# Kernel optimization log

Measured on AMD Instinct MI355X. Metric: run time of the kernel, lower is better.

## Reference

```python
import jax, jax.numpy as jnp
import numpy as np

B, N, D, L, T = 64, 64, 6, 32, 2048
RHO = 0.7
W = np.float32(RHO ** (1.0 / L))  # per-step decay, rho ** (1/l_patts)


def setup_inputs() -> dict:
    key = jax.random.key(0)
    k1, k2 = jax.random.split(key)
    x = jax.random.normal(k1, (B, D, T), dtype=jnp.float32)
    patts = jax.random.normal(k2, (N, L), dtype=jnp.float32)  # torch.randn(n_patts, l_patts)
    w = jnp.float32(W)
    return {"x": x, "patts": patts, "w": w}


def _dtw_sq(x, patts, w):
    """Open-end (subsequence) weighted DTW of each pattern against each channel.

    DP recurrence (squared-distance cost, decay w on accumulated path):
      D[0, j] = c[0, j]                                    (free start in time)
      D[i, j] = c[i, j] + w * min(D[i-1, j], D[i, j-1], D[i-1, j-1])
    Output O[b, n, d, j] = D[L-1, j]  (distance of full pattern ending at time j).
    """
    b, d, t = x.shape
    n, l = patts.shape
    is_first = jnp.arange(l) == 0  # (L,)

    def col_step(Dprev_t, xt):
        # Dprev_t: (L, B, N, D) previous time column; xt: (B, D)
        # cost c[i] = (patts[n, i] - x[b, d, j])^2 -> (L, B, N, D)
        c_t = (patts.T[:, None, :, None] - xt[None, :, None, :]) ** 2
        Dprev_im1 = jnp.concatenate(
            [jnp.full_like(Dprev_t[:1], jnp.inf), Dprev_t[:-1]], axis=0)

        def cell(d_im1, inputs):
            ci, dp_i, dp_im1, first = inputs
            m = jnp.minimum(jnp.minimum(dp_i, dp_im1), d_im1)
            di = jnp.where(first, ci, ci + w * m)
            return di, di

        init = jnp.full(Dprev_t.shape[1:], jnp.inf, x.dtype)
        _, Dcol_t = jax.lax.scan(cell, init, (c_t, Dprev_t, Dprev_im1, is_first))
        return Dcol_t, Dcol_t[-1]  # carry full column, emit last row D[L-1, j]

    Dinit = jnp.full((l, b, n, d), jnp.inf, x.dtype)
    xs = jnp.moveaxis(x, -1, 0)  # (T, B, D)
    _, last = jax.lax.scan(col_step, Dinit, xs)  # (T, B, N, D)
    return jnp.moveaxis(last, 0, -1)  # (B, N, D, T)


def reference(x, patts, w):
    return jnp.sqrt(_dtw_sq(x, patts, w))
```

## Files before the change

### kernel.cpp

```cpp
#include <hip/hip_runtime.h>
#include <math.h>

#define TB 2048
#define LL 32
#define NP 64
#define DD 6
#define BB 64
#define NLANES 8
#define ROWS 4
#define PAD 8


template<bool CHECK>
__device__ __forceinline__ void dtw_step(
    int s, int k, bool k0, bool k7,
    const float* __restrict__ xp, float w,
    float p0, float p1, float p2, float p3,
    float& cur0, float& cur1, float& cur2, float& cur3,
    float& diag, float* __restrict__ orow)
{
    const float INF = __builtin_inff();
    float up = __shfl_up(cur3, 1, 64);
    float xv = xp[s];
    int j = s - k;
    bool valid = true;
    if (CHECK) valid = ((unsigned)j < (unsigned)TB);

    float c0 = p0 - xv; c0 *= c0;
    float c1 = p1 - xv; c1 *= c1;
    float c2 = p2 - xv; c2 *= c2;
    float c3 = p3 - xv; c3 *= c3;

    float m0 = fminf(fminf(cur0, up), diag);
    float v0 = k0 ? c0 : fmaf(w, m0, c0);
    float n0 = (CHECK && !valid) ? INF : v0;
    float m1 = fminf(fminf(cur1, n0), cur0);
    float v1 = fmaf(w, m1, c1);
    float n1 = (CHECK && !valid) ? INF : v1;
    float m2 = fminf(fminf(cur2, n1), cur1);
    float v2 = fmaf(w, m2, c2);
    float n2 = (CHECK && !valid) ? INF : v2;
    float m3 = fminf(fminf(cur3, n2), cur2);
    float v3 = fmaf(w, m3, c3);
    float n3 = (CHECK && !valid) ? INF : v3;

    diag = up;
    cur0 = n0; cur1 = n1; cur2 = n2; cur3 = n3;

    if (k7) {
        if (!CHECK || valid) orow[j] = sqrtf(n3);
    }
}

__global__ __launch_bounds__(256) void dtw_kernel(
    const float* __restrict__ x,
    const float* __restrict__ patts,
    const float* __restrict__ wptr,
    float* __restrict__ out)
{
    __shared__ float xs[PAD + TB + PAD];

    const int bid  = blockIdx.x;
    const int half = bid & 1;
    const int bd   = bid >> 1;
    const int b    = bd / DD;
    const int d    = bd - b * DD;
    const int tid  = threadIdx.x;

    const float4* xrow = (const float4*)(x + (size_t)bd * TB);
    float4* xs4 = (float4*)(xs + PAD);
    xs4[tid]       = xrow[tid];
    xs4[tid + 256] = xrow[tid + 256];
    if (tid < PAD) { xs[tid] = 0.f; xs[PAD + TB + tid] = 0.f; }
    __syncthreads();

    const int g = tid >> 3;
    const int k = tid & 7;
    const int n = half * 32 + g;

    const float w = wptr[0];
    const float4 pv = *(const float4*)(patts + n * LL + k * ROWS);
    const float p0 = pv.x, p1 = pv.y, p2 = pv.z, p3 = pv.w;

    float* orow = out + (((size_t)b * NP + n) * DD + d) * TB;
    const float* xp = xs + PAD - k;

    const float INF = __builtin_inff();
    float cur0 = INF, cur1 = INF, cur2 = INF, cur3 = INF, diag = INF;
    const bool k0 = (k == 0), k7 = (k == NLANES - 1);

    int s = 0;
    for (; s < NLANES - 1; ++s)
        dtw_step<true>(s, k, k0, k7, xp, w, p0, p1, p2, p3,
                       cur0, cur1, cur2, cur3, diag, orow);
    #pragma unroll 4
    for (; s < TB; ++s)
        dtw_step<false>(s, k, k0, k7, xp, w, p0, p1, p2, p3,
                        cur0, cur1, cur2, cur3, diag, orow);
    for (; s < TB + NLANES - 1; ++s)
        dtw_step<true>(s, k, k0, k7, xp, w, p0, p1, p2, p3,
                       cur0, cur1, cur2, cur3, diag, orow);
}

extern "C" void kernel_launch(void* const* d_in, const int* in_sizes, int n_in,
                              void* d_out, int out_size, void* d_ws, size_t ws_size,
                              hipStream_t stream) {
    const float* x     = (const float*)d_in[0];
    const float* patts = (const float*)d_in[1];
    const float* wptr  = (const float*)d_in[2];
    float* out = (float*)d_out;

    dim3 grid(BB * DD * 2);
    dim3 block(256);
    dtw_kernel<<<grid, block, 0, stream>>>(x, patts, wptr, out);
}
```

Baseline: 357.0 us.

## Skew DTW wavefront by 16-step time chunks instead of single steps

The lane-to-lane wavefront now advances one 16-column chunk at a time instead of one column at a time. Each chunk's boundary values are exchanged with 16 independent shuffles at its start, so shuffle latency no longer sits on the critical path of every step. Outputs are written as float4 stores. In exchange, pipeline fill and drain grow to seven chunks, adding some redundant compute. Register use also rises because of the 16-entry boundary arrays.

```diff
diff --git a/kernel.cpp b/kernel.cpp
--- a/kernel.cpp
+++ b/kernel.cpp
@@ -8,49 +8,9 @@
 #define BB 64
 #define NLANES 8
 #define ROWS 4
-#define PAD 8
+#define CW 16
+#define MSTEPS (TB/CW)
 
-
-template<bool CHECK>
-__device__ __forceinline__ void dtw_step(
-    int s, int k, bool k0, bool k7,
-    const float* __restrict__ xp, float w,
-    float p0, float p1, float p2, float p3,
-    float& cur0, float& cur1, float& cur2, float& cur3,
-    float& diag, float* __restrict__ orow)
-{
-    const float INF = __builtin_inff();
-    float up = __shfl_up(cur3, 1, 64);
-    float xv = xp[s];
-    int j = s - k;
-    bool valid = true;
-    if (CHECK) valid = ((unsigned)j < (unsigned)TB);
-
-    float c0 = p0 - xv; c0 *= c0;
-    float c1 = p1 - xv; c1 *= c1;
-    float c2 = p2 - xv; c2 *= c2;
-    float c3 = p3 - xv; c3 *= c3;
-
-    float m0 = fminf(fminf(cur0, up), diag);
-    float v0 = k0 ? c0 : fmaf(w, m0, c0);
-    float n0 = (CHECK && !valid) ? INF : v0;
-    float m1 = fminf(fminf(cur1, n0), cur0);
-    float v1 = fmaf(w, m1, c1);
-    float n1 = (CHECK && !valid) ? INF : v1;
-    float m2 = fminf(fminf(cur2, n1), cur1);
-    float v2 = fmaf(w, m2, c2);
-    float n2 = (CHECK && !valid) ? INF : v2;
-    float m3 = fminf(fminf(cur3, n2), cur2);
-    float v3 = fmaf(w, m3, c3);
-    float n3 = (CHECK && !valid) ? INF : v3;
-
-    diag = up;
-    cur0 = n0; cur1 = n1; cur2 = n2; cur3 = n3;
-
-    if (k7) {
-        if (!CHECK || valid) orow[j] = sqrtf(n3);
-    }
-}
 
 __global__ __launch_bounds__(256) void dtw_kernel(
     const float* __restrict__ x,
@@ -58,20 +18,17 @@
     const float* __restrict__ wptr,
     float* __restrict__ out)
 {
-    __shared__ float xs[PAD + TB + PAD];
+    __shared__ float xs[TB];
 
     const int bid  = blockIdx.x;
     const int half = bid & 1;
     const int bd   = bid >> 1;
-    const int b    = bd / DD;
-    const int d    = bd - b * DD;
     const int tid  = threadIdx.x;
 
     const float4* xrow = (const float4*)(x + (size_t)bd * TB);
-    float4* xs4 = (float4*)(xs + PAD);
+    float4* xs4 = (float4*)xs;
     xs4[tid]       = xrow[tid];
     xs4[tid + 256] = xrow[tid + 256];
-    if (tid < PAD) { xs[tid] = 0.f; xs[PAD + TB + tid] = 0.f; }
     __syncthreads();
 
     const int g = tid >> 3;
@@ -82,24 +39,64 @@
     const float4 pv = *(const float4*)(patts + n * LL + k * ROWS);
     const float p0 = pv.x, p1 = pv.y, p2 = pv.z, p3 = pv.w;
 
-    float* orow = out + (((size_t)b * NP + n) * DD + d) * TB;
-    const float* xp = xs + PAD - k;
+    const int b = bd / DD, d = bd - (bd / DD) * DD;
+    float* __restrict__ orow = out + (((size_t)b * NP + n) * DD + d) * TB;
 
+    const bool k0 = (k == 0), k7 = (k == NLANES - 1);
     const float INF = __builtin_inff();
-    float cur0 = INF, cur1 = INF, cur2 = INF, cur3 = INF, diag = INF;
-    const bool k0 = (k == 0), k7 = (k == NLANES - 1);
 
-    int s = 0;
-    for (; s < NLANES - 1; ++s)
-        dtw_step<true>(s, k, k0, k7, xp, w, p0, p1, p2, p3,
-                       cur0, cur1, cur2, cur3, diag, orow);
-    #pragma unroll 4
-    for (; s < TB; ++s)
-        dtw_step<false>(s, k, k0, k7, xp, w, p0, p1, p2, p3,
-                        cur0, cur1, cur2, cur3, diag, orow);
-    for (; s < TB + NLANES - 1; ++s)
-        dtw_step<true>(s, k, k0, k7, xp, w, p0, p1, p2, p3,
-                       cur0, cur1, cur2, cur3, diag, orow);
+    float a0 = INF, a1 = INF, a2 = INF, a3 = INF;
+    float diagC = INF;
+    float r3[CW];
+    #pragma unroll
+    for (int c = 0; c < CW; ++c) r3[c] = INF;
+
+    for (int m = 0; m < MSTEPS + NLANES - 1; ++m) {
+        const int q = m - k;
+        const bool valid = ((unsigned)q < (unsigned)MSTEPS);
+
+        float recv[CW];
+        #pragma unroll
+        for (int c = 0; c < CW; ++c) recv[c] = __shfl_up(r3[c], 1, 64);
+
+        const int qq = valid ? q : 0;
+        const float4* xq = (const float4*)(xs + qq * CW);
+        const float4 xA = xq[0], xB = xq[1], xC = xq[2], xD = xq[3];
+        const float xv[CW] = {xA.x, xA.y, xA.z, xA.w,  xB.x, xB.y, xB.z, xB.w,
+                              xC.x, xC.y, xC.z, xC.w,  xD.x, xD.y, xD.z, xD.w};
+
+        float diag = diagC;
+        #pragma unroll
+        for (int c = 0; c < CW; ++c) {
+            const float xvc = xv[c];
+            float t0 = p0 - xvc, t1 = p1 - xvc, t2 = p2 - xvc, t3 = p3 - xvc;
+            const float c0 = t0 * t0, c1 = t1 * t1, c2 = t2 * t2, c3 = t3 * t3;
+            const float up = recv[c];
+            const float l0 = a0, l1 = a1, l2 = a2, l3 = a3;
+
+            const float m0 = fminf(fminf(l0, up), diag);
+            const float v0 = k0 ? c0 : fmaf(w, m0, c0);
+            const float m1 = fminf(fminf(l1, v0), l0);
+            const float v1 = fmaf(w, m1, c1);
+            const float m2 = fminf(fminf(l2, v1), l1);
+            const float v2 = fmaf(w, m2, c2);
+            const float m3 = fminf(fminf(l3, v2), l2);
+            const float v3 = fmaf(w, m3, c3);
+
+            a0 = v0; a1 = v1; a2 = v2; a3 = v3;
+            diag = up;
+            r3[c] = v3;
+        }
+        diagC = diag;
+
+        if (k7 && valid) {
+            float4* op = (float4*)(orow + q * CW);
+            op[0] = make_float4(sqrtf(r3[0]),  sqrtf(r3[1]),  sqrtf(r3[2]),  sqrtf(r3[3]));
+            op[1] = make_float4(sqrtf(r3[4]),  sqrtf(r3[5]),  sqrtf(r3[6]),  sqrtf(r3[7]));
+            op[2] = make_float4(sqrtf(r3[8]),  sqrtf(r3[9]),  sqrtf(r3[10]), sqrtf(r3[11]));
+            op[3] = make_float4(sqrtf(r3[12]), sqrtf(r3[13]), sqrtf(r3[14]), sqrtf(r3[15]));
+        }
+    }
 }
 
 extern "C" void kernel_launch(void* const* d_in, const int* in_sizes, int n_in,
```

Measured after the change: 304.6 us. 14.7% less time.
